# Kernel optimization log

Hardware: AMD Instinct MI355X
Metric: run time of the kernel (lower is better)

## Reference

```python
import jax, jax.numpy as jnp
import numpy as np

N, E, K, F_IN, H = 50000, 640000, 3, 128, 128


def setup_inputs() -> dict:
    key = jax.random.key(0)
    ks = jax.random.split(key, 14)
    s = 0.05
    return {
        "x": jax.random.normal(ks[0], (N, F_IN), jnp.float32),
        "edge_index": jax.random.randint(ks[1], (2, E), 0, N, dtype=jnp.int32),
        "edge_weight": jax.random.uniform(ks[2], (E,), jnp.float32, minval=0.1, maxval=1.0),
        "W_x": jax.random.normal(ks[3], (4, F_IN, H), jnp.float32) * s,   # dense input weights (i,f,c,o)
        "w_c": jax.random.normal(ks[4], (3, H), jnp.float32) * s,         # peephole weights (i,f,o)
        "b": jax.random.normal(ks[5], (4, H), jnp.float32) * s,           # gate biases (i,f,c,o)
        "theta": jax.random.normal(ks[6], (4, K, H, H), jnp.float32) * s, # ChebConv weights per gate
        "theta_b": jax.random.normal(ks[7], (4, H), jnp.float32) * s,     # ChebConv biases per gate
        "gcn_w": jax.random.normal(ks[8], (H, H), jnp.float32) * s,
        "gcn_b": jnp.zeros((H,), jnp.float32),
        "bn_gamma": jnp.ones((H,), jnp.float32),
        "bn_beta": jnp.zeros((H,), jnp.float32),
        "bn_mean": jax.random.normal(ks[9], (H,), jnp.float32) * 0.1,
        "bn_var": jax.random.uniform(ks[10], (H,), jnp.float32, minval=0.5, maxval=1.5),
        "lin_w": jax.random.normal(ks[11], (H, 1), jnp.float32) * s,
        "lin_b": jnp.zeros((1,), jnp.float32),
    }


def reference(x, edge_index, edge_weight, W_x, w_c, b, theta, theta_b, gcn_w, gcn_b, bn_gamma, bn_beta, bn_mean, bn_var, lin_w, lin_b):
    n = x.shape[0]
    src, dst = edge_index[0], edge_index[1]

    # --- ChebConv normalization (sym, lambda_max=2): L_hat = -D^{-1/2} A D^{-1/2}, zero diagonal ---
    deg = jnp.zeros((n,), x.dtype).at[src].add(edge_weight)
    safe = jnp.where(deg > 0, deg, 1.0)
    dis = jnp.where(deg > 0, jax.lax.rsqrt(safe), 0.0)
    lw = -dis[src] * edge_weight * dis[dst]  # per-edge scaled-Laplacian weight

    def prop(h):  # out[i] = sum_{edges j->i} lw * h[j]
        return jnp.zeros_like(h).at[dst].add(lw[:, None] * h[src])

    def cheb(h, th, tb):  # sum_k T_k(L_hat) h @ theta_k + bias, Chebyshev recurrence
        Tx0, out = h, h @ th[0]
        Tx1 = prop(h)
        out = out + Tx1 @ th[1]
        for k in range(2, K):
            Tx2 = 2.0 * prop(Tx1) - Tx0
            out = out + Tx2 @ th[k]
            Tx0, Tx1 = Tx1, Tx2
        return out + tb

    # --- GCLSTM with H = C = 0 (module passes no initial state) ---
    Hs = jnp.zeros((n, W_x.shape[2]), x.dtype)
    Cs = jnp.zeros_like(Hs)
    I = jax.nn.sigmoid(x @ W_x[0] + cheb(Hs, theta[0], theta_b[0]) + w_c[0] * Cs + b[0])
    Fg = jax.nn.sigmoid(x @ W_x[1] + cheb(Hs, theta[1], theta_b[1]) + w_c[1] * Cs + b[1])
    T = jnp.tanh(x @ W_x[2] + cheb(Hs, theta[2], theta_b[2]) + b[2])
    Cs = Fg * Cs + I * T
    O = jax.nn.sigmoid(x @ W_x[3] + cheb(Hs, theta[3], theta_b[3]) + w_c[2] * Cs + b[3])
    Hs = O * jnp.tanh(Cs)

    # --- GCNConv(H) with unit edge weights + added self-loops ---
    h = Hs @ gcn_w
    deg_g = jnp.ones((n,), x.dtype).at[dst].add(jnp.ones((edge_index.shape[1],), x.dtype))
    dg = jax.lax.rsqrt(deg_g)
    g = jnp.zeros_like(h).at[dst].add((dg[src] * dg[dst])[:, None] * h[src]) + (dg * dg)[:, None] * h + gcn_b

    g = jax.nn.relu(g)
    g = bn_gamma * (g - bn_mean) * jax.lax.rsqrt(bn_var + 1e-5) + bn_beta  # BatchNorm1d (eval)
    return g @ lin_w + lin_b  # Dropout = identity in eval
```

## Files before the change

kernel.cpp:

```cpp
#include <hip/hip_runtime.h>
#include <hip/hip_bf16.h>

#define NN 50000
#define NE 640000
#define NZB 196
#define CAP 64
#define NGB 782
#define NFB 625

typedef unsigned short ushort_t;
typedef unsigned int uint_t;
typedef __attribute__((ext_vector_type(8))) short bf16x8;
typedef __attribute__((ext_vector_type(4))) float f32x4;

__device__ __forceinline__ float b2f(ushort_t u) {
    union { uint_t u; float f; } v; v.u = ((uint_t)u) << 16; return v.f;
}
__device__ __forceinline__ ushort_t f2b(float f) {
    union { float f; uint_t u; } v; v.f = f;
    uint_t u = v.u;
    uint_t r = u + 0x7fffu + ((u >> 16) & 1u);
    return (ushort_t)(r >> 16);
}
__device__ __forceinline__ float fsig(float x)  { return __builtin_amdgcn_rcpf(1.0f + __expf(-x)); }
__device__ __forceinline__ float ftanh(float x) { return 1.0f - 2.0f * __builtin_amdgcn_rcpf(1.0f + __expf(2.0f * x)); }
__device__ __forceinline__ float ldm(const void* p, int i, int mf) {
    return mf ? ((const float*)p)[i] : b2f(((const ushort_t*)p)[i]);
}

#define CSH 4
#define OFF_HB   0
#define OFF_BSRC 12800000
#define OFF_CNT  25600000
#define OFF_WT   28800000
#define OFF_COEF 28931072
#define OFF_MODE 28933636
#define WS_REQ   28933640

__global__ void fb_k(ushort_t* __restrict__ out, int n) {
    int i = blockIdx.x * blockDim.x + threadIdx.x;
    if (i < n) out[i] = 0;
}

__global__ void prep_k(const ushort_t* __restrict__ x,
                       const void* __restrict__ Wx, const void* __restrict__ gcnw,
                       const void* __restrict__ wc, const void* __restrict__ bb,
                       const void* __restrict__ thb,
                       const void* __restrict__ gam, const void* __restrict__ bet,
                       const void* __restrict__ mea, const void* __restrict__ var,
                       const void* __restrict__ linw, const void* __restrict__ linb,
                       ushort_t* __restrict__ WT, float* __restrict__ coef,
                       int* __restrict__ cnt, int* __restrict__ mode) {
    __shared__ int si[256];
    __shared__ float red[128];
    int b = blockIdx.x, t = threadIdx.x;
    if (b < NZB) {
        int i = b * 256 + t;
        if (i < NN) cnt[i << CSH] = 0;
        return;
    }
    int bad = 0;
    for (int i = t; i < 4096; i += 256) {
        int e = (x[i] >> 7) & 0xFF;
        if (e >= 0xC0) bad++;
    }
    si[t] = bad; __syncthreads();
    for (int o = 128; o >= 1; o >>= 1) { if (t < o) si[t] += si[t + o]; __syncthreads(); }
    int mf = (si[0] > 8) ? 1 : 0;

    int wb = b - NZB;
    if (wb < 32) {
        int gid = wb * 256 + t;
        int m  = gid >> 11;
        int u  = gid & 2047;
        int k  = u >> 4;
        int f0 = (u & 15) << 3;
        const int srcoff[4] = { 0, 2 * 16384, 3 * 16384, 0 };
        const void* S = (m == 3) ? gcnw : Wx;
        int sbase = srcoff[m] + k * 128 + f0;
        ushort_t vals[8];
        if (mf == 0) {
            bf16x8 v = *(const bf16x8*)((const ushort_t*)S + sbase);
            #pragma unroll
            for (int i = 0; i < 8; i++) vals[i] = (ushort_t)v[i];
        } else {
            const float* Sf = (const float*)S + sbase;
            #pragma unroll
            for (int i = 0; i < 8; i++) vals[i] = f2b(Sf[i]);
        }
        ushort_t* D = WT + m * 16384 + k;
        #pragma unroll
        for (int i = 0; i < 8; i++) D[(f0 + i) * 128] = vals[i];
    } else {
        if (t < 128) {
            float rs = rsqrtf(ldm(var, t, mf) + 1e-5f);
            float ga = ldm(gam, t, mf);
            float lw = ldm(linw, t, mf);
            coef[t]       = ldm(thb, t, mf)           + ldm(bb, t, mf);
            coef[128 + t] = ldm(thb, 2 * 128 + t, mf) + ldm(bb, 2 * 128 + t, mf);
            coef[256 + t] = ldm(thb, 3 * 128 + t, mf) + ldm(bb, 3 * 128 + t, mf);
            coef[384 + t] = ldm(wc, 2 * 128 + t, mf);
            coef[512 + t] = ga * rs * lw;
            red[t] = (ldm(bet, t, mf) - ldm(mea, t, mf) * ga * rs) * lw;
        }
        __syncthreads();
        for (int off = 64; off >= 1; off >>= 1) {
            if (t < off && t < 128) red[t] += red[t + off];
            __syncthreads();
        }
        if (t == 0) {
            coef[640] = red[0] + ldm(linb, 0, mf);
            mode[0] = mf;
        }
    }
}

__launch_bounds__(256)
__global__ void gafi_k(const void* __restrict__ x, const ushort_t* __restrict__ WT,
                       const float* __restrict__ coef, const int* __restrict__ mode,
                       ushort_t* __restrict__ hb,
                       const int* __restrict__ ei, int* __restrict__ cnt,
                       int* __restrict__ bsrc) {
    __shared__ ushort_t tile[64 * 136];
    int per = blockIdx.x / 9, rem = blockIdx.x % 9;
    int t = threadIdx.x;

    if (rem >= 5) {
        int fb = per * 4 + (rem - 5);
        if (fb >= NFB) return;
        int tid = fb * 256 + t;
        int4 s4 = ((const int4*)ei)[tid];
        int4 d4 = ((const int4*)(ei + NE))[tid];
        int p0 = atomicAdd(&cnt[d4.x << CSH], 1);
        int p1 = atomicAdd(&cnt[d4.y << CSH], 1);
        int p2 = atomicAdd(&cnt[d4.z << CSH], 1);
        int p3 = atomicAdd(&cnt[d4.w << CSH], 1);
        if (p0 < CAP) bsrc[d4.x * CAP + p0] = s4.x;
        if (p1 < CAP) bsrc[d4.y * CAP + p1] = s4.y;
        if (p2 < CAP) bsrc[d4.z * CAP + p2] = s4.z;
        if (p3 < CAP) bsrc[d4.w * CAP + p3] = s4.w;
        return;
    }

    int gb = per * 5 + rem;
    if (gb >= NGB) return;
    int base = gb * 64;
    int mf = mode[0];

    for (int i = 0; i < 4; i++) {
        int idx = (i * 256 + t) * 8;
        int row = idx >> 7, col = idx & 127;
        int n = base + row;
        bf16x8 v;
        if (n >= NN) {
            v = (bf16x8)0;
        } else if (mf == 0) {
            v = *(const bf16x8*)((const ushort_t*)x + n * 128 + col);
        } else {
            const float* xf = (const float*)x + n * 128 + col;
            float4 lo = *(const float4*)xf;
            float4 hi = *(const float4*)(xf + 4);
            v[0] = (short)f2b(lo.x); v[1] = (short)f2b(lo.y);
            v[2] = (short)f2b(lo.z); v[3] = (short)f2b(lo.w);
            v[4] = (short)f2b(hi.x); v[5] = (short)f2b(hi.y);
            v[6] = (short)f2b(hi.z); v[7] = (short)f2b(hi.w);
        }
        *(bf16x8*)&tile[row * 136 + col] = v;
    }
    __syncthreads();

    int lane = t & 63, wave = t >> 6;
    int m = lane & 15, quad = lane >> 4;

    bf16x8 a[4][4];
    #pragma unroll
    for (int rt = 0; rt < 4; rt++)
        #pragma unroll
        for (int kt = 0; kt < 4; kt++)
            a[rt][kt] = *(const bf16x8*)&tile[(rt * 16 + m) * 136 + kt * 32 + quad * 8];
    __syncthreads();

    const ushort_t* WTi = WT;
    const ushort_t* WTc = WT + 16384;
    const ushort_t* WTo = WT + 2 * 16384;

    #pragma unroll
    for (int ft = 0; ft < 2; ft++) {
        int f = wave * 32 + ft * 16 + m;
        bf16x8 bi[4], bc[4], bo[4];
        #pragma unroll
        for (int kt = 0; kt < 4; kt++) {
            int off = f * 128 + kt * 32 + quad * 8;
            bi[kt] = *(const bf16x8*)(WTi + off);
            bc[kt] = *(const bf16x8*)(WTc + off);
            bo[kt] = *(const bf16x8*)(WTo + off);
        }
        float bi_f = coef[f], bc_f = coef[128 + f], bo_f = coef[256 + f], w2 = coef[384 + f];
        #pragma unroll
        for (int rt = 0; rt < 4; rt++) {
            f32x4 ai = {0,0,0,0}, ac = {0,0,0,0}, ao = {0,0,0,0};
            #pragma unroll
            for (int kt = 0; kt < 4; kt++) {
                ai = __builtin_amdgcn_mfma_f32_16x16x32_bf16(a[rt][kt], bi[kt], ai, 0, 0, 0);
                ac = __builtin_amdgcn_mfma_f32_16x16x32_bf16(a[rt][kt], bc[kt], ac, 0, 0, 0);
                ao = __builtin_amdgcn_mfma_f32_16x16x32_bf16(a[rt][kt], bo[kt], ao, 0, 0, 0);
            }
            #pragma unroll
            for (int r = 0; r < 4; r++) {
                float I  = fsig(ai[r] + bi_f);
                float T  = ftanh(ac[r] + bc_f);
                float Cs = I * T;
                float O  = fsig(ao[r] + w2 * Cs + bo_f);
                float Hs = O * ftanh(Cs);
                tile[(rt * 16 + quad * 4 + r) * 136 + f] = f2b(Hs);
            }
        }
    }
    __syncthreads();

    const ushort_t* WTg = WT + 3 * 16384;
    bf16x8 ah[4][4];
    #pragma unroll
    for (int rt = 0; rt < 4; rt++)
        #pragma unroll
        for (int kt = 0; kt < 4; kt++)
            ah[rt][kt] = *(const bf16x8*)&tile[(rt * 16 + m) * 136 + kt * 32 + quad * 8];

    #pragma unroll
    for (int ft = 0; ft < 2; ft++) {
        int f = wave * 32 + ft * 16 + m;
        bf16x8 bg[4];
        #pragma unroll
        for (int kt = 0; kt < 4; kt++)
            bg[kt] = *(const bf16x8*)(WTg + f * 128 + kt * 32 + quad * 8);
        #pragma unroll
        for (int rt = 0; rt < 4; rt++) {
            f32x4 acc = {0,0,0,0};
            #pragma unroll
            for (int kt = 0; kt < 4; kt++)
                acc = __builtin_amdgcn_mfma_f32_16x16x32_bf16(ah[rt][kt], bg[kt], acc, 0, 0, 0);
            #pragma unroll
            for (int r = 0; r < 4; r++) {
                int n = base + rt * 16 + quad * 4 + r;
                if (n < NN) hb[n * 128 + f] = f2b(acc[r]);
            }
        }
    }
}

__launch_bounds__(256)
__global__ void gat_out_k(const ushort_t* __restrict__ hb, const int* __restrict__ cnt,
                          const int* __restrict__ bsrc,
                          const void* __restrict__ gcnb, const float* __restrict__ coef,
                          const int* __restrict__ mode, void* __restrict__ out) {
    int wid  = (blockIdx.x * blockDim.x + threadIdx.x) >> 6;
    int lane = threadIdx.x & 63;
    if (wid >= NN) return;
    int half = lane >> 5, sl = lane & 31;
    int c = cnt[wid << CSH]; if (c < 0) c = 0;
    int deg = (c < CAP) ? c : CAP;
    const int* brow = bsrc + wid * CAP;

    float a0 = 0.0f, a1 = 0.0f, a2 = 0.0f, a3 = 0.0f;
    int s0 = brow[half];
    int s1 = brow[half + 2];
    for (int j = half; j < deg; j += 4) {
        int sn0 = brow[(j + 4) & (CAP - 1)];
        int sn1 = brow[(j + 6) & (CAP - 1)];
        {
            int cs = cnt[s0 << CSH]; if (cs < 0) cs = 0;
            uint2 r = *(const uint2*)(hb + s0 * 128 + sl * 4);
            float w = rsqrtf(1.0f + (float)cs);
            a0 += w * b2f((ushort_t)(r.x & 0xffffu));
            a1 += w * b2f((ushort_t)(r.x >> 16));
            a2 += w * b2f((ushort_t)(r.y & 0xffffu));
            a3 += w * b2f((ushort_t)(r.y >> 16));
        }
        if (j + 2 < deg) {
            int cs = cnt[s1 << CSH]; if (cs < 0) cs = 0;
            uint2 r = *(const uint2*)(hb + s1 * 128 + sl * 4);
            float w = rsqrtf(1.0f + (float)cs);
            a0 += w * b2f((ushort_t)(r.x & 0xffffu));
            a1 += w * b2f((ushort_t)(r.x >> 16));
            a2 += w * b2f((ushort_t)(r.y & 0xffffu));
            a3 += w * b2f((ushort_t)(r.y >> 16));
        }
        s0 = sn0; s1 = sn1;
    }
    float d = rsqrtf(1.0f + (float)c);
    if (half == 0) {
        uint2 r = *(const uint2*)(hb + wid * 128 + sl * 4);
        a0 += d * b2f((ushort_t)(r.x & 0xffffu));
        a1 += d * b2f((ushort_t)(r.x >> 16));
        a2 += d * b2f((ushort_t)(r.y & 0xffffu));
        a3 += d * b2f((ushort_t)(r.y >> 16));
    }
    a0 += __shfl_xor(a0, 32); a1 += __shfl_xor(a1, 32);
    a2 += __shfl_xor(a2, 32); a3 += __shfl_xor(a3, 32);
    int mf = mode[0];
    int fb = sl * 4;
    float g0 = d * a0 + ldm(gcnb, fb,     mf);
    float g1 = d * a1 + ldm(gcnb, fb + 1, mf);
    float g2 = d * a2 + ldm(gcnb, fb + 2, mf);
    float g3 = d * a3 + ldm(gcnb, fb + 3, mf);
    float v = fmaxf(g0, 0.0f) * coef[512 + fb]
            + fmaxf(g1, 0.0f) * coef[512 + fb + 1]
            + fmaxf(g2, 0.0f) * coef[512 + fb + 2]
            + fmaxf(g3, 0.0f) * coef[512 + fb + 3];
    #pragma unroll
    for (int o = 32; o >= 1; o >>= 1) v += __shfl_down(v, o);
    if (lane == 0) {
        float r = 0.5f * v + coef[640];
        if (mf) ((float*)out)[wid] = r;
        else    ((ushort_t*)out)[wid] = f2b(r);
    }
}

extern "C" void kernel_launch(void* const* d_in, const int* in_sizes, int n_in,
                              void* d_out, int out_size, void* d_ws, size_t ws_size,
                              hipStream_t stream) {
    if (ws_size < (size_t)WS_REQ) {
        fb_k<<<(out_size + 255) / 256, 256, 0, stream>>>((ushort_t*)d_out, out_size);
        return;
    }
    const void* x    = d_in[0];
    const int*  ei   = (const int*)d_in[1];
    const void* Wx   = d_in[3];
    const void* wc   = d_in[4];
    const void* bb   = d_in[5];
    const void* thb  = d_in[7];
    const void* gcnw = d_in[8];
    const void* gcnb = d_in[9];
    const void* gam  = d_in[10];
    const void* bet  = d_in[11];
    const void* mea  = d_in[12];
    const void* var  = d_in[13];
    const void* linw = d_in[14];
    const void* linb = d_in[15];

    char* ws = (char*)d_ws;
    ushort_t* hb   = (ushort_t*)(ws + OFF_HB);
    int*      bsrc = (int*)     (ws + OFF_BSRC);
    int*      cnt  = (int*)     (ws + OFF_CNT);
    ushort_t* WT   = (ushort_t*)(ws + OFF_WT);
    float*    coef = (float*)   (ws + OFF_COEF);
    int*      mode = (int*)     (ws + OFF_MODE);

    prep_k<<<NZB + 33, 256, 0, stream>>>((const ushort_t*)x, Wx, gcnw, wc, bb, thb,
                                         gam, bet, mea, var, linw, linb, WT, coef, cnt, mode);
    gafi_k<<<157 * 9, 256, 0, stream>>>(x, WT, coef, mode, hb, ei, cnt, bsrc);
    gat_out_k<<<(NN * 64 + 255) / 256, 256, 0, stream>>>(hb, cnt, bsrc, gcnb, coef, mode, d_out);
}
```

Before: 187.9 us.

## Replace global atomic edge bucketing with two-pass shared-memory binned counting sort

Global-atomic per-destination bucketing in the fused kernel is replaced by a two-pass scheme. The first pass bins edges by groups of 64 destination nodes, using shared-memory histograms and prefix sums per edge chunk. A new scatter kernel then gathers each bin's segments from every chunk, builds the per-node neighbor lists in LDS and writes them out with coalesced stores. This removes contended, scattered global atomics and the padded count array, and the separate zeroing pass is no longer needed. The cost is an extra kernel launch and an extra pass over the edge data through a staging buffer.

Measured after the change: 177.6 us. -5.5%, faster.

```diff
diff --git a/kernel.cpp b/kernel.cpp
--- a/kernel.cpp
+++ b/kernel.cpp
@@ -3,10 +3,12 @@
 
 #define NN 50000
 #define NE 640000
-#define NZB 196
 #define CAP 64
 #define NGB 782
-#define NFB 625
+#define NBIN 782
+#define NA 196
+#define EPA 3328
+#define ORow 784
 
 typedef unsigned short ushort_t;
 typedef unsigned int uint_t;
@@ -28,14 +30,15 @@
     return mf ? ((const float*)p)[i] : b2f(((const ushort_t*)p)[i]);
 }
 
-#define CSH 4
-#define OFF_HB   0
-#define OFF_BSRC 12800000
-#define OFF_CNT  25600000
-#define OFF_WT   28800000
-#define OFF_COEF 28931072
-#define OFF_MODE 28933636
-#define WS_REQ   28933640
+#define OFF_HB    0
+#define OFF_BSRC  12800000
+#define OFF_CNT   25600000
+#define OFF_CHUNK 25800000
+#define OFF_OFFS  28409152
+#define OFF_WT    29023808
+#define OFF_COEF  29154880
+#define OFF_MODE  29157444
+#define WS_REQ    29157448
 
 __global__ void fb_k(ushort_t* __restrict__ out, int n) {
     int i = blockIdx.x * blockDim.x + threadIdx.x;
@@ -50,15 +53,10 @@
                        const void* __restrict__ mea, const void* __restrict__ var,
                        const void* __restrict__ linw, const void* __restrict__ linb,
                        ushort_t* __restrict__ WT, float* __restrict__ coef,
-                       int* __restrict__ cnt, int* __restrict__ mode) {
+                       int* __restrict__ mode) {
     __shared__ int si[256];
     __shared__ float red[128];
     int b = blockIdx.x, t = threadIdx.x;
-    if (b < NZB) {
-        int i = b * 256 + t;
-        if (i < NN) cnt[i << CSH] = 0;
-        return;
-    }
     int bad = 0;
     for (int i = t; i < 4096; i += 256) {
         int e = (x[i] >> 7) & 0xFF;
@@ -68,9 +66,8 @@
     for (int o = 128; o >= 1; o >>= 1) { if (t < o) si[t] += si[t + o]; __syncthreads(); }
     int mf = (si[0] > 8) ? 1 : 0;
 
-    int wb = b - NZB;
-    if (wb < 32) {
-        int gid = wb * 256 + t;
+    if (b < 32) {
+        int gid = b * 256 + t;
         int m  = gid >> 11;
         int u  = gid & 2047;
         int k  = u >> 4;
@@ -119,30 +116,58 @@
 __global__ void gafi_k(const void* __restrict__ x, const ushort_t* __restrict__ WT,
                        const float* __restrict__ coef, const int* __restrict__ mode,
                        ushort_t* __restrict__ hb,
-                       const int* __restrict__ ei, int* __restrict__ cnt,
-                       int* __restrict__ bsrc) {
-    __shared__ ushort_t tile[64 * 136];
-    int per = blockIdx.x / 9, rem = blockIdx.x % 9;
+                       const int* __restrict__ ei, uint_t* __restrict__ chunk,
+                       int* __restrict__ offs) {
+    __shared__ int sh[4352];
+    ushort_t* tile = (ushort_t*)sh;
+    int per = blockIdx.x / 5, rem = blockIdx.x % 5;
     int t = threadIdx.x;
 
-    if (rem >= 5) {
-        int fb = per * 4 + (rem - 5);
-        if (fb >= NFB) return;
-        int tid = fb * 256 + t;
-        int4 s4 = ((const int4*)ei)[tid];
-        int4 d4 = ((const int4*)(ei + NE))[tid];
-        int p0 = atomicAdd(&cnt[d4.x << CSH], 1);
-        int p1 = atomicAdd(&cnt[d4.y << CSH], 1);
-        int p2 = atomicAdd(&cnt[d4.z << CSH], 1);
-        int p3 = atomicAdd(&cnt[d4.w << CSH], 1);
-        if (p0 < CAP) bsrc[d4.x * CAP + p0] = s4.x;
-        if (p1 < CAP) bsrc[d4.y * CAP + p1] = s4.y;
-        if (p2 < CAP) bsrc[d4.z * CAP + p2] = s4.z;
-        if (p3 < CAP) bsrc[d4.w * CAP + p3] = s4.w;
+    if (rem == 4) {
+        int a = per;
+        int e0 = a * EPA; if (e0 > NE) e0 = NE;
+        int e1 = e0 + EPA; if (e1 > NE) e1 = NE;
+        const int* dstp = ei + NE;
+        for (int i = t; i < NBIN; i += 256) sh[i] = 0;
+        __syncthreads();
+        for (int i = e0 + t; i < e1; i += 256) atomicAdd(&sh[dstp[i] >> 6], 1);
+        __syncthreads();
+        int b0 = t * 4;
+        int s = 0;
+        #pragma unroll
+        for (int j = 0; j < 4; j++) { int bi = b0 + j; if (bi < NBIN) s += sh[bi]; }
+        sh[1024 + t] = s;
+        __syncthreads();
+        for (int off = 1; off < 256; off <<= 1) {
+            int v = (t >= off) ? sh[1024 + t - off] : 0;
+            __syncthreads();
+            sh[1024 + t] += v;
+            __syncthreads();
+        }
+        int run = (t == 0) ? 0 : sh[1024 + t - 1];
+        int* orow = offs + a * ORow;
+        #pragma unroll
+        for (int j = 0; j < 4; j++) {
+            int bi = b0 + j;
+            if (bi < NBIN) {
+                int c = sh[bi];
+                orow[bi] = run;
+                sh[bi] = run;
+                run += c;
+            }
+        }
+        if (t == 0) orow[NBIN] = e1 - e0;
+        __syncthreads();
+        uint_t* ck = chunk + a * EPA;
+        for (int i = e0 + t; i < e1; i += 256) {
+            int d = dstp[i], sn = ei[i];
+            int pos = atomicAdd(&sh[d >> 6], 1);
+            ck[pos] = ((uint_t)sn << 6) | (uint_t)(d & 63);
+        }
         return;
     }
 
-    int gb = per * 5 + rem;
+    int gb = per * 4 + rem;
     if (gb >= NGB) return;
     int base = gb * 64;
     int mf = mode[0];
@@ -249,6 +274,52 @@
 }
 
 __launch_bounds__(256)
+__global__ void scat_k(const uint_t* __restrict__ chunk, const int* __restrict__ offs,
+                       int* __restrict__ bsrc, int* __restrict__ cnt) {
+    __shared__ int sstart[NA];
+    __shared__ int P[256];
+    __shared__ int lcnt[64];
+    __shared__ uint_t lbuck[64 * CAP];
+    int b = blockIdx.x, t = threadIdx.x;
+    int node0 = b << 6;
+    if (t < 64) lcnt[t] = 0;
+    int len = 0;
+    if (t < NA) {
+        int st = offs[t * ORow + b];
+        int en = offs[t * ORow + b + 1];
+        sstart[t] = st;
+        len = en - st;
+    }
+    P[t] = len;
+    __syncthreads();
+    for (int off = 1; off < 256; off <<= 1) {
+        int v = (t >= off) ? P[t - off] : 0;
+        __syncthreads();
+        P[t] += v;
+        __syncthreads();
+    }
+    int T = P[255];
+    for (int i = t; i < T; i += 256) {
+        int lo = 0, hi = NA - 1;
+        while (lo < hi) { int mid = (lo + hi) >> 1; if (P[mid] > i) hi = mid; else lo = mid + 1; }
+        int prev = (lo == 0) ? 0 : P[lo - 1];
+        uint_t w = chunk[lo * EPA + sstart[lo] + (i - prev)];
+        int d6 = (int)(w & 63u);
+        int sn = (int)(w >> 6);
+        int p = atomicAdd(&lcnt[d6], 1);
+        if (p < CAP) lbuck[(d6 << 6) + p] = (uint_t)sn;
+    }
+    __syncthreads();
+    if (t < 64) { int node = node0 + t; if (node < NN) cnt[node] = lcnt[t]; }
+    const int4* lb4 = (const int4*)lbuck;
+    int4* bs4 = (int4*)bsrc;
+    for (int i = t; i < 1024; i += 256) {
+        int node = node0 + (i >> 4);
+        if (node < NN) bs4[(node0 << 4) + i] = lb4[i];
+    }
+}
+
+__launch_bounds__(256)
 __global__ void gat_out_k(const ushort_t* __restrict__ hb, const int* __restrict__ cnt,
                           const int* __restrict__ bsrc,
                           const void* __restrict__ gcnb, const float* __restrict__ coef,
@@ -257,7 +328,7 @@
     int lane = threadIdx.x & 63;
     if (wid >= NN) return;
     int half = lane >> 5, sl = lane & 31;
-    int c = cnt[wid << CSH]; if (c < 0) c = 0;
+    int c = cnt[wid]; if (c < 0) c = 0;
     int deg = (c < CAP) ? c : CAP;
     const int* brow = bsrc + wid * CAP;
 
@@ -268,7 +339,7 @@
         int sn0 = brow[(j + 4) & (CAP - 1)];
         int sn1 = brow[(j + 6) & (CAP - 1)];
         {
-            int cs = cnt[s0 << CSH]; if (cs < 0) cs = 0;
+            int cs = cnt[s0]; if (cs < 0) cs = 0;
             uint2 r = *(const uint2*)(hb + s0 * 128 + sl * 4);
             float w = rsqrtf(1.0f + (float)cs);
             a0 += w * b2f((ushort_t)(r.x & 0xffffu));
@@ -277,7 +348,7 @@
             a3 += w * b2f((ushort_t)(r.y >> 16));
         }
         if (j + 2 < deg) {
-            int cs = cnt[s1 << CSH]; if (cs < 0) cs = 0;
+            int cs = cnt[s1]; if (cs < 0) cs = 0;
             uint2 r = *(const uint2*)(hb + s1 * 128 + sl * 4);
             float w = rsqrtf(1.0f + (float)cs);
             a0 += w * b2f((ushort_t)(r.x & 0xffffu));
@@ -339,15 +410,18 @@
     const void* linb = d_in[15];
 
     char* ws = (char*)d_ws;
-    ushort_t* hb   = (ushort_t*)(ws + OFF_HB);
-    int*      bsrc = (int*)     (ws + OFF_BSRC);
-    int*      cnt  = (int*)     (ws + OFF_CNT);
-    ushort_t* WT   = (ushort_t*)(ws + OFF_WT);
-    float*    coef = (float*)   (ws + OFF_COEF);
-    int*      mode = (int*)     (ws + OFF_MODE);
-
-    prep_k<<<NZB + 33, 256, 0, stream>>>((const ushort_t*)x, Wx, gcnw, wc, bb, thb,
-                                         gam, bet, mea, var, linw, linb, WT, coef, cnt, mode);
-    gafi_k<<<157 * 9, 256, 0, stream>>>(x, WT, coef, mode, hb, ei, cnt, bsrc);
+    ushort_t* hb    = (ushort_t*)(ws + OFF_HB);
+    int*      bsrc  = (int*)     (ws + OFF_BSRC);
+    int*      cnt   = (int*)     (ws + OFF_CNT);
+    uint_t*   chunk = (uint_t*)  (ws + OFF_CHUNK);
+    int*      offs  = (int*)     (ws + OFF_OFFS);
+    ushort_t* WT    = (ushort_t*)(ws + OFF_WT);
+    float*    coef  = (float*)   (ws + OFF_COEF);
+    int*      mode  = (int*)     (ws + OFF_MODE);
+
+    prep_k<<<33, 256, 0, stream>>>((const ushort_t*)x, Wx, gcnw, wc, bb, thb,
+                                   gam, bet, mea, var, linw, linb, WT, coef, mode);
+    gafi_k<<<NA * 5, 256, 0, stream>>>(x, WT, coef, mode, hb, ei, chunk, offs);
+    scat_k<<<NBIN, 256, 0, stream>>>(chunk, offs, bsrc, cnt);
     gat_out_k<<<(NN * 64 + 255) / 256, 256, 0, stream>>>(hb, cnt, bsrc, gcnb, coef, mode, d_out);
 }
```
